# Kernel optimization log

Hardware: AMD Instinct MI355X
Metric: run time of the kernel (lower is better)

Reference implementation:

```python
import jax, jax.numpy as jnp
import numpy as np

D = 3            # input_ch (pos dims)
L = 16           # n_levels
F = 2            # n_feats per level
LOG2 = 19
CAP = 1 << LOG2  # hashmap capacity per level
COARSEST, FINEST = 16.0, 2048.0
N = 524288
D1 = D + 1
HASH_MULT = np.int32(2531011)


def _elevate_matrix():
    # Linear map R^D -> hyperplane {sum=0} in R^{D+1} (Adams et al. permutohedral lattice)
    sf = 1.0 / np.sqrt(np.arange(1, D + 1, dtype=np.float64) * np.arange(2, D + 2, dtype=np.float64))
    E = np.zeros((D1, D), np.float32)
    E[0, :] = sf
    for i in range(1, D1):
        E[i, i - 1] = -i * sf[i - 1]
        E[i, i:] = sf[i:]
    return E


def _scales():
    g = (FINEST / COARSEST) ** (np.arange(L, dtype=np.float64) / (L - 1))
    return (COARSEST * g).astype(np.float32)


def permuto_forward(pos, params):
    E = jnp.asarray(_elevate_matrix())
    scales = jnp.asarray(_scales())
    x = pos[None] * scales[:, None, None]              # [L,N,D]
    elev = jnp.einsum('vp,lnp->lnv', E, x)             # [L,N,D1]
    # nearest lattice remainder-0 point (multiples of D1)
    rem0f = jnp.round(elev / D1) * D1
    sums = (jnp.sum(rem0f, -1) / D1).astype(jnp.int32)  # exactly integer
    di = elev - rem0f
    # rank[i] = #{j : d_j > d_i  or (d_j == d_i and j < i)}
    gt = di[..., None, :] > di[..., :, None]
    eq = di[..., None, :] == di[..., :, None]
    jlt = jnp.arange(D1)[None, :] < jnp.arange(D1)[:, None]
    rank = jnp.sum(gt | (eq & jlt), -1).astype(jnp.int32) + sums[..., None]
    rem0 = rem0f.astype(jnp.int32)
    under = (rank < 0).astype(jnp.int32)
    over = (rank > D).astype(jnp.int32)
    rank = rank + (under - over) * D1
    rem0 = rem0 + (under - over) * D1
    # barycentric weights of the D1 simplex vertices
    delta = (elev - rem0.astype(elev.dtype)) / D1      # [L,N,D1]
    dbr = jnp.take_along_axis(delta, jnp.argsort(rank, -1), -1)  # delta ordered by rank
    w0 = 1.0 + dbr[..., -1] - dbr[..., 0]
    w = jnp.concatenate([w0[..., None], -(dbr[..., 1:] - dbr[..., :-1])[..., ::-1]], -1)  # [L,N,D1]
    # integer keys of the D1 simplex vertices (first D coords; last is implicit)
    kk = jnp.arange(D1, dtype=jnp.int32)
    keys = (rem0[..., None, :D] + kk[:, None]
            - D1 * (rank[..., None, :D] > (D - kk[:, None])).astype(jnp.int32))  # [L,N,D1,D]
    # hash: k = (k + key_i) * 2531011, wrap in 32 bits, mask to capacity (pow2)
    h = jnp.zeros(keys.shape[:-1], jnp.int32)
    for i in range(D):
        h = (h + keys[..., i]) * HASH_MULT
    idx = h & (CAP - 1)                                # [L,N,D1]
    flat_idx = idx + jnp.arange(L, dtype=jnp.int32)[:, None, None] * CAP
    feats = params.reshape(L * CAP, F)[flat_idx]       # [L,N,D1,F]
    out = jnp.einsum('lnv,lnvf->lnf', w, feats)        # [L,N,F]
    return jnp.moveaxis(out, 0, 1).reshape(pos.shape[0], L * F)


def setup_inputs() -> dict:
    key = jax.random.key(0)
    k1, k2 = jax.random.split(key)
    pos = jax.random.uniform(k1, (N, D), jnp.float32)                 # coords in [0,1)
    params = jax.random.normal(k2, (L * CAP * F,), jnp.float32) * 1e-4  # param_init std
    return {"input": pos, "flattened_params": params}


def reference(input, flattened_params):
    return permuto_forward(input, flattened_params)
```

## Files before the change

### kernel.cpp

```cpp
#include <hip/hip_runtime.h>
#include <hip/hip_fp16.h>
#include <cmath>

namespace {

typedef float    vf4 __attribute__((ext_vector_type(4)));
typedef unsigned uv2 __attribute__((ext_vector_type(2)));

constexpr int kN = 524288;
constexpr int kL = 16;
constexpr int kCapLog2 = 19;
constexpr int kCap = 1 << kCapLog2;
constexpr int kCapMask = kCap - 1;
constexpr unsigned kHashMult = 2531011u;

constexpr int cD[4][3]   = {{ 8, 8, 6},{10,10, 9},{13,12,10},{17,16,14}};
constexpr int cB[4][3]   = {{-4,-16,-16},{-4,-20,-24},{-4,-24,-28},{-4,-32,-40}};
constexpr int cCnt[4]    = {1536, 3600, 6240, 15232};
constexpr int cOff[4]    = {0, 1536, 5136, 11376};
constexpr int kLdsCnt    = 11376;
constexpr int kDenseCnt  = 26608;

struct ScaleArr { float s[kL]; };

__device__ __forceinline__ void permuto_point(
    float x0, float x1, float x2, int rem0[4], int rank[4], float w[4])
{
    const float E00 = (float)( 0.70710678118654752440);
    const float E01 = (float)( 0.40824829046386301637);
    const float E02 = (float)( 0.28867513459481288225);
    const float E10 = (float)(-0.70710678118654752440);
    const float E21 = (float)(-2.0 * 0.40824829046386301637);
    const float E32 = (float)(-3.0 * 0.28867513459481288225);

    float elev[4];
    elev[0] = E00 * x0 + E01 * x1 + E02 * x2;
    elev[1] = E10 * x0 + E01 * x1 + E02 * x2;
    elev[2] =            E21 * x1 + E02 * x2;
    elev[3] =                       E32 * x2;

    float rem0f[4], di[4];
    #pragma unroll
    for (int v = 0; v < 4; ++v) {
        rem0f[v] = rintf(elev[v] * 0.25f) * 4.0f;
        di[v]    = elev[v] - rem0f[v];
    }
    const int sums = (int)((((rem0f[0] + rem0f[1]) + rem0f[2]) + rem0f[3]) * 0.25f);

    #pragma unroll
    for (int a = 0; a < 4; ++a) {
        int r = 0;
        #pragma unroll
        for (int b = 0; b < 4; ++b)
            r += (di[b] > di[a]) || (di[b] == di[a] && b < a);
        rank[a] = r + sums;
        rem0[a] = (int)rem0f[a];
    }
    #pragma unroll
    for (int v = 0; v < 4; ++v) {
        if (rank[v] < 0)      { rank[v] += 4; rem0[v] += 4; }
        else if (rank[v] > 3) { rank[v] -= 4; rem0[v] -= 4; }
    }

    float dbr[4];
    #pragma unroll
    for (int v = 0; v < 4; ++v)
        dbr[rank[v] & 3] = (elev[v] - (float)rem0[v]) * 0.25f;

    w[0] = (1.0f + dbr[3]) - dbr[0];
    w[1] = dbr[2] - dbr[3];
    w[2] = dbr[1] - dbr[2];
    w[3] = dbr[0] - dbr[1];
}

__global__ __launch_bounds__(256) void conv_tab(const float* __restrict__ params,
                                                unsigned* __restrict__ tab)
{
    const int i = blockIdx.x * 256 + threadIdx.x;
    vf4 v = __builtin_nontemporal_load((const vf4*)params + i);
    __half2 a = __floats2half2_rn(v.x, v.y);
    __half2 b = __floats2half2_rn(v.z, v.w);
    uv2 o;
    o.x = *reinterpret_cast<unsigned*>(&a);
    o.y = *reinterpret_cast<unsigned*>(&b);
    __builtin_nontemporal_store(o, (uv2*)tab + i);
}

__global__ __launch_bounds__(256) void build_dense(const float* __restrict__ params,
                                                   unsigned* __restrict__ dense)
{
    const int e = blockIdx.x * 256 + threadIdx.x;
    if (e >= kDenseCnt) return;
    int l, r;
    if      (e < cOff[1]) { l = 0; r = e; }
    else if (e < cOff[2]) { l = 1; r = e - cOff[1]; }
    else if (e < cOff[3]) { l = 2; r = e - cOff[2]; }
    else                  { l = 3; r = e - cOff[3]; }
    const int d0 = cD[l][0], d1 = cD[l][1], d2 = cD[l][2];
    const int per = d0 * d1 * d2;
    const int k  = r / per;  r -= k * per;
    const int i0 = r / (d1 * d2); r -= i0 * (d1 * d2);
    const int i1 = r / d2;
    const int i2 = r - i1 * d2;

    const int key0 = cB[l][0] + 4 * i0 + k;
    const int key1 = cB[l][1] + 4 * i1 + k;
    const int key2 = cB[l][2] + 4 * i2 + k;
    int h = 0;
    h = (int)((unsigned)(h + key0) * kHashMult);
    h = (int)((unsigned)(h + key1) * kHashMult);
    h = (int)((unsigned)(h + key2) * kHashMult);
    const size_t entry = ((size_t)l << kCapLog2) + (h & kCapMask);
    const __half2 hv = __floats2half2_rn(params[entry * 2], params[entry * 2 + 1]);
    dense[e] = *reinterpret_cast<const unsigned*>(&hv);
}

__global__ __launch_bounds__(256) void permuto_coarse(
    const float* __restrict__ pos,
    const unsigned* __restrict__ dense,
    unsigned* __restrict__ out_t16,
    ScaleArr sc)
{
    __shared__ unsigned sd[kLdsCnt];
    for (int i = threadIdx.x; i < kLdsCnt; i += 256)
        sd[i] = dense[i];
    __syncthreads();

    const int n = blockIdx.x * 256 + threadIdx.x;
    const float p0 = __builtin_nontemporal_load(pos + 3 * n + 0);
    const float p1 = __builtin_nontemporal_load(pos + 3 * n + 1);
    const float p2 = __builtin_nontemporal_load(pos + 3 * n + 2);
    const unsigned* __restrict__ denseL3 = dense + cOff[3];

    #pragma unroll
    for (int l = 0; l < 4; ++l) {
        const float s = sc.s[l];
        int rem0[4], rank[4];
        float w[4];
        permuto_point(p0 * s, p1 * s, p2 * s, rem0, rank, w);

        unsigned ev[4];
        #pragma unroll
        for (int k = 0; k < 4; ++k) {
            const int i0 = (rem0[0] - 4 * (rank[0] > 3 - k) - cB[l][0]) >> 2;
            const int i1 = (rem0[1] - 4 * (rank[1] > 3 - k) - cB[l][1]) >> 2;
            const int i2 = (rem0[2] - 4 * (rank[2] > 3 - k) - cB[l][2]) >> 2;
            const int idx = ((k * cD[l][0] + i0) * cD[l][1] + i1) * cD[l][2] + i2;
            ev[k] = (l < 3) ? sd[cOff[l] + idx] : denseL3[idx];
        }
        float o0 = 0.0f, o1 = 0.0f;
        #pragma unroll
        for (int k = 0; k < 4; ++k) {
            const __half2 hv = *reinterpret_cast<const __half2*>(&ev[k]);
            o0 += w[k] * __low2float(hv);
            o1 += w[k] * __high2float(hv);
        }
        const __half2 po = __floats2half2_rn(o0, o1);
        __builtin_nontemporal_store(*reinterpret_cast<const unsigned*>(&po),
                                    out_t16 + ((size_t)l << kCapLog2) + n);
    }
}

__global__ __launch_bounds__(256) void permuto_fine(
    const float* __restrict__ pos,
    const unsigned* __restrict__ tab,
    unsigned* __restrict__ out_t16,
    ScaleArr sc)
{
    const int b   = blockIdx.x;
    const int xcd = b & 7;
    const int j   = b >> 3;
    int level, n;
    if (j < 2048) {
        level = 4 + xcd;
        n = (j << 8) + threadIdx.x;
    } else {
        level = 12 + (xcd & 3);
        const int c = ((j - 2048) << 1) | (xcd >> 2);
        n = (c << 8) + threadIdx.x;
    }

    const float s  = sc.s[level];
    const float x0 = __builtin_nontemporal_load(pos + 3 * n + 0) * s;
    const float x1 = __builtin_nontemporal_load(pos + 3 * n + 1) * s;
    const float x2 = __builtin_nontemporal_load(pos + 3 * n + 2) * s;

    int rem0[4], rank[4];
    float w[4];
    permuto_point(x0, x1, x2, rem0, rank, w);

    const unsigned* __restrict__ t = tab + ((size_t)level << kCapLog2);
    int hidx[4];
    #pragma unroll
    for (int k = 0; k < 4; ++k) {
        int h = 0;
        #pragma unroll
        for (int i = 0; i < 3; ++i) {
            const int key = rem0[i] + k - 4 * (rank[i] > 3 - k);
            h = (int)((unsigned)(h + key) * kHashMult);
        }
        hidx[k] = h & kCapMask;
    }
    unsigned e[4];
    #pragma unroll
    for (int k = 0; k < 4; ++k) e[k] = t[hidx[k]];

    float o0 = 0.0f, o1 = 0.0f;
    #pragma unroll
    for (int k = 0; k < 4; ++k) {
        const __half2 hv = *reinterpret_cast<const __half2*>(&e[k]);
        o0 += w[k] * __low2float(hv);
        o1 += w[k] * __high2float(hv);
    }
    const __half2 po = __floats2half2_rn(o0, o1);
    __builtin_nontemporal_store(*reinterpret_cast<const unsigned*>(&po),
                                out_t16 + ((size_t)level << kCapLog2) + n);
}

__global__ __launch_bounds__(256) void transpose_out16(
    const unsigned* __restrict__ out_t16, vf4* __restrict__ out4)
{
    __shared__ float tile[256][36];
    const int t  = threadIdx.x;
    const int p0 = blockIdx.x * 256;

    #pragma unroll
    for (int l = 0; l < kL; ++l) {
        const unsigned u = __builtin_nontemporal_load(out_t16 + ((size_t)l << kCapLog2) + p0 + t);
        const __half2 hv = *reinterpret_cast<const __half2*>(&u);
        tile[t][2 * l + 0] = __low2float(hv);
        tile[t][2 * l + 1] = __high2float(hv);
    }
    __syncthreads();

    const size_t base = (size_t)p0 * 8;
    #pragma unroll
    for (int i = 0; i < 8; ++i) {
        const int idx = i * 256 + t;
        const int p = idx >> 3, q = idx & 7;
        vf4 v = *reinterpret_cast<const vf4*>(&tile[p][4 * q]);
        out4[base + idx] = v;
    }
}

__global__ __launch_bounds__(256) void permuto_fwd(
    const float* __restrict__ pos,
    const float* __restrict__ params,
    float* __restrict__ out,
    ScaleArr sc)
{
    const int gid = blockIdx.x * 256 + threadIdx.x;
    const int l = gid & (kL - 1);
    const int n = gid >> 4;

    const float s  = sc.s[l];
    const float x0 = pos[3 * n + 0] * s;
    const float x1 = pos[3 * n + 1] * s;
    const float x2 = pos[3 * n + 2] * s;

    int rem0[4], rank[4];
    float w[4];
    permuto_point(x0, x1, x2, rem0, rank, w);

    const float2* __restrict__ tab = (const float2*)params + ((size_t)l << kCapLog2);
    float o0 = 0.0f, o1 = 0.0f;
    #pragma unroll
    for (int k = 0; k < 4; ++k) {
        int h = 0;
        #pragma unroll
        for (int i = 0; i < 3; ++i) {
            const int key = rem0[i] + k - 4 * (rank[i] > 3 - k);
            h = (int)((unsigned)(h + key) * kHashMult);
        }
        const float2 f = tab[h & kCapMask];
        o0 += w[k] * f.x;
        o1 += w[k] * f.y;
    }
    ((float2*)out)[(n << 4) + l] = make_float2(o0, o1);
}

}

extern "C" void kernel_launch(void* const* d_in, const int* in_sizes, int n_in,
                              void* d_out, int out_size, void* d_ws, size_t ws_size,
                              hipStream_t stream) {
    const float* pos    = (const float*)d_in[0];
    const float* params = (const float*)d_in[1];
    float* out          = (float*)d_out;

    ScaleArr sc;
    for (int l = 0; l < kL; ++l)
        sc.s[l] = (float)(16.0 * pow(128.0, (double)l / 15.0));

    const size_t tab_bytes   = (size_t)kL * kCap * 4;
    const size_t outt_bytes  = (size_t)kL * kN * 4;
    const size_t dense_bytes = (size_t)kDenseCnt * 4;

    if (ws_size >= tab_bytes + outt_bytes + dense_bytes) {
        unsigned* tab     = (unsigned*)d_ws;
        unsigned* out_t16 = (unsigned*)((char*)d_ws + tab_bytes);
        unsigned* dense   = (unsigned*)((char*)d_ws + tab_bytes + outt_bytes);

        conv_tab<<<(kL * kCap * 2 / 4) / 256, 256, 0, stream>>>(params, tab);
        build_dense<<<(kDenseCnt + 255) / 256, 256, 0, stream>>>(params, dense);
        permuto_coarse<<<kN / 256, 256, 0, stream>>>(pos, dense, out_t16, sc);
        permuto_fine<<<8 * 3072, 256, 0, stream>>>(pos, tab, out_t16, sc);
        transpose_out16<<<kN / 256, 256, 0, stream>>>(out_t16, (vf4*)out);
    } else {
        permuto_fwd<<<(kN * kL) / 256, 256, 0, stream>>>(pos, params, out, sc);
    }
}
```

Before: 186.3 us.

## Fuse table conversion with fp32 gathers for levels 4-6 into one kernel

```diff
diff --git a/kernel.cpp b/kernel.cpp
--- a/kernel.cpp
+++ b/kernel.cpp
@@ -16,10 +16,13 @@
 
 constexpr int cD[4][3]   = {{ 8, 8, 6},{10,10, 9},{13,12,10},{17,16,14}};
 constexpr int cB[4][3]   = {{-4,-16,-16},{-4,-20,-24},{-4,-24,-28},{-4,-32,-40}};
-constexpr int cCnt[4]    = {1536, 3600, 6240, 15232};
 constexpr int cOff[4]    = {0, 1536, 5136, 11376};
 constexpr int kLdsCnt    = 11376;
 constexpr int kDenseCnt  = 26608;
+
+constexpr int kMegaMain  = 15360;
+constexpr int kBuildBlks = 104;
+constexpr int kConvBaseF4 = 7 * (kCap * 2 / 4);
 
 struct ScaleArr { float s[kL]; };
 
@@ -73,46 +76,149 @@
     w[3] = dbr[0] - dbr[1];
 }
 
-__global__ __launch_bounds__(256) void conv_tab(const float* __restrict__ params,
-                                                unsigned* __restrict__ tab)
-{
-    const int i = blockIdx.x * 256 + threadIdx.x;
-    vf4 v = __builtin_nontemporal_load((const vf4*)params + i);
-    __half2 a = __floats2half2_rn(v.x, v.y);
-    __half2 b = __floats2half2_rn(v.z, v.w);
-    uv2 o;
-    o.x = *reinterpret_cast<unsigned*>(&a);
-    o.y = *reinterpret_cast<unsigned*>(&b);
-    __builtin_nontemporal_store(o, (uv2*)tab + i);
-}
-
-__global__ __launch_bounds__(256) void build_dense(const float* __restrict__ params,
-                                                   unsigned* __restrict__ dense)
-{
-    const int e = blockIdx.x * 256 + threadIdx.x;
-    if (e >= kDenseCnt) return;
-    int l, r;
-    if      (e < cOff[1]) { l = 0; r = e; }
-    else if (e < cOff[2]) { l = 1; r = e - cOff[1]; }
-    else if (e < cOff[3]) { l = 2; r = e - cOff[2]; }
-    else                  { l = 3; r = e - cOff[3]; }
-    const int d0 = cD[l][0], d1 = cD[l][1], d2 = cD[l][2];
-    const int per = d0 * d1 * d2;
-    const int k  = r / per;  r -= k * per;
-    const int i0 = r / (d1 * d2); r -= i0 * (d1 * d2);
-    const int i1 = r / d2;
-    const int i2 = r - i1 * d2;
-
-    const int key0 = cB[l][0] + 4 * i0 + k;
-    const int key1 = cB[l][1] + 4 * i1 + k;
-    const int key2 = cB[l][2] + 4 * i2 + k;
-    int h = 0;
-    h = (int)((unsigned)(h + key0) * kHashMult);
-    h = (int)((unsigned)(h + key1) * kHashMult);
-    h = (int)((unsigned)(h + key2) * kHashMult);
-    const size_t entry = ((size_t)l << kCapLog2) + (h & kCapMask);
-    const __half2 hv = __floats2half2_rn(params[entry * 2], params[entry * 2 + 1]);
-    dense[e] = *reinterpret_cast<const unsigned*>(&hv);
+__global__ __launch_bounds__(256) void mega1(
+    const float* __restrict__ pos,
+    const float* __restrict__ params,
+    unsigned* __restrict__ tab,
+    unsigned* __restrict__ out_t16,
+    unsigned* __restrict__ dense,
+    ScaleArr sc)
+{
+    const int b = blockIdx.x;
+    if (b < kMegaMain) {
+        const int q = b / 5, r = b % 5;
+        if (r < 2) {
+            const int idx   = q * 2 + r;
+            const int level = 4 + (idx >> 11);
+            const int n     = ((idx & 2047) << 8) + threadIdx.x;
+
+            const float s  = sc.s[level];
+            const float x0 = __builtin_nontemporal_load(pos + 3 * n + 0) * s;
+            const float x1 = __builtin_nontemporal_load(pos + 3 * n + 1) * s;
+            const float x2 = __builtin_nontemporal_load(pos + 3 * n + 2) * s;
+
+            int rem0[4], rank[4];
+            float w[4];
+            permuto_point(x0, x1, x2, rem0, rank, w);
+
+            const float2* __restrict__ t2 =
+                (const float2*)params + ((size_t)level << kCapLog2);
+            int hidx[4];
+            #pragma unroll
+            for (int k = 0; k < 4; ++k) {
+                int h = 0;
+                #pragma unroll
+                for (int i = 0; i < 3; ++i) {
+                    const int key = rem0[i] + k - 4 * (rank[i] > 3 - k);
+                    h = (int)((unsigned)(h + key) * kHashMult);
+                }
+                hidx[k] = h & kCapMask;
+            }
+            float2 f[4];
+            #pragma unroll
+            for (int k = 0; k < 4; ++k) f[k] = t2[hidx[k]];
+
+            float o0 = 0.0f, o1 = 0.0f;
+            #pragma unroll
+            for (int k = 0; k < 4; ++k) { o0 += w[k] * f[k].x; o1 += w[k] * f[k].y; }
+
+            const __half2 po = __floats2half2_rn(o0, o1);
+            __builtin_nontemporal_store(*reinterpret_cast<const unsigned*>(&po),
+                                        out_t16 + ((size_t)level << kCapLog2) + n);
+        } else {
+            const int i  = q * 3 + (r - 2);
+            const int jj = kConvBaseF4 + i * 256 + threadIdx.x;
+            vf4 v = __builtin_nontemporal_load((const vf4*)params + jj);
+            __half2 a = __floats2half2_rn(v.x, v.y);
+            __half2 c = __floats2half2_rn(v.z, v.w);
+            uv2 o;
+            o.x = *reinterpret_cast<unsigned*>(&a);
+            o.y = *reinterpret_cast<unsigned*>(&c);
+            __builtin_nontemporal_store(o, (uv2*)tab + jj);
+        }
+    } else {
+        const int e = (b - kMegaMain) * 256 + threadIdx.x;
+        if (e >= kDenseCnt) return;
+        int l, r;
+        if      (e < cOff[1]) { l = 0; r = e; }
+        else if (e < cOff[2]) { l = 1; r = e - cOff[1]; }
+        else if (e < cOff[3]) { l = 2; r = e - cOff[2]; }
+        else                  { l = 3; r = e - cOff[3]; }
+        const int d0 = cD[l][0], d1 = cD[l][1], d2 = cD[l][2];
+        const int per = d0 * d1 * d2;
+        int rr = r;
+        const int k  = rr / per;  rr -= k * per;
+        const int i0 = rr / (d1 * d2); rr -= i0 * (d1 * d2);
+        const int i1 = rr / d2;
+        const int i2 = rr - i1 * d2;
+
+        const int key0 = cB[l][0] + 4 * i0 + k;
+        const int key1 = cB[l][1] + 4 * i1 + k;
+        const int key2 = cB[l][2] + 4 * i2 + k;
+        int h = 0;
+        h = (int)((unsigned)(h + key0) * kHashMult);
+        h = (int)((unsigned)(h + key1) * kHashMult);
+        h = (int)((unsigned)(h + key2) * kHashMult);
+        const size_t entry = ((size_t)l << kCapLog2) + (h & kCapMask);
+        const __half2 hv = __floats2half2_rn(params[entry * 2], params[entry * 2 + 1]);
+        dense[e] = *reinterpret_cast<const unsigned*>(&hv);
+    }
+}
+
+__global__ __launch_bounds__(256) void fine715(
+    const float* __restrict__ pos,
+    const unsigned* __restrict__ tab,
+    unsigned* __restrict__ out_t16,
+    ScaleArr sc)
+{
+    const int b   = blockIdx.x;
+    const int xcd = b & 7;
+    const int j   = b >> 3;
+    int level, n;
+    if (j < 2048) {
+        level = 7 + xcd;
+        n = (j << 8) + threadIdx.x;
+    } else {
+        level = 15;
+        const int c = (j - 2048) + (xcd << 8);
+        n = (c << 8) + threadIdx.x;
+    }
+
+    const float s  = sc.s[level];
+    const float x0 = __builtin_nontemporal_load(pos + 3 * n + 0) * s;
+    const float x1 = __builtin_nontemporal_load(pos + 3 * n + 1) * s;
+    const float x2 = __builtin_nontemporal_load(pos + 3 * n + 2) * s;
+
+    int rem0[4], rank[4];
+    float w[4];
+    permuto_point(x0, x1, x2, rem0, rank, w);
+
+    const unsigned* __restrict__ t = tab + ((size_t)level << kCapLog2);
+    int hidx[4];
+    #pragma unroll
+    for (int k = 0; k < 4; ++k) {
+        int h = 0;
+        #pragma unroll
+        for (int i = 0; i < 3; ++i) {
+            const int key = rem0[i] + k - 4 * (rank[i] > 3 - k);
+            h = (int)((unsigned)(h + key) * kHashMult);
+        }
+        hidx[k] = h & kCapMask;
+    }
+    unsigned e[4];
+    #pragma unroll
+    for (int k = 0; k < 4; ++k) e[k] = t[hidx[k]];
+
+    float o0 = 0.0f, o1 = 0.0f;
+    #pragma unroll
+    for (int k = 0; k < 4; ++k) {
+        const __half2 hv = *reinterpret_cast<const __half2*>(&e[k]);
+        o0 += w[k] * __low2float(hv);
+        o1 += w[k] * __high2float(hv);
+    }
+    const __half2 po = __floats2half2_rn(o0, o1);
+    __builtin_nontemporal_store(*reinterpret_cast<const unsigned*>(&po),
+                                out_t16 + ((size_t)level << kCapLog2) + n);
 }
 
 __global__ __launch_bounds__(256) void permuto_coarse(
@@ -161,62 +267,6 @@
     }
 }
 
-__global__ __launch_bounds__(256) void permuto_fine(
-    const float* __restrict__ pos,
-    const unsigned* __restrict__ tab,
-    unsigned* __restrict__ out_t16,
-    ScaleArr sc)
-{
-    const int b   = blockIdx.x;
-    const int xcd = b & 7;
-    const int j   = b >> 3;
-    int level, n;
-    if (j < 2048) {
-        level = 4 + xcd;
-        n = (j << 8) + threadIdx.x;
-    } else {
-        level = 12 + (xcd & 3);
-        const int c = ((j - 2048) << 1) | (xcd >> 2);
-        n = (c << 8) + threadIdx.x;
-    }
-
-    const float s  = sc.s[level];
-    const float x0 = __builtin_nontemporal_load(pos + 3 * n + 0) * s;
-    const float x1 = __builtin_nontemporal_load(pos + 3 * n + 1) * s;
-    const float x2 = __builtin_nontemporal_load(pos + 3 * n + 2) * s;
-
-    int rem0[4], rank[4];
-    float w[4];
-    permuto_point(x0, x1, x2, rem0, rank, w);
-
-    const unsigned* __restrict__ t = tab + ((size_t)level << kCapLog2);
-    int hidx[4];
-    #pragma unroll
-    for (int k = 0; k < 4; ++k) {
-        int h = 0;
-        #pragma unroll
-        for (int i = 0; i < 3; ++i) {
-            const int key = rem0[i] + k - 4 * (rank[i] > 3 - k);
-            h = (int)((unsigned)(h + key) * kHashMult);
-        }
-        hidx[k] = h & kCapMask;
-    }
-    unsigned e[4];
-    #pragma unroll
-    for (int k = 0; k < 4; ++k) e[k] = t[hidx[k]];
-
-    float o0 = 0.0f, o1 = 0.0f;
-    #pragma unroll
-    for (int k = 0; k < 4; ++k) {
-        const __half2 hv = *reinterpret_cast<const __half2*>(&e[k]);
-        o0 += w[k] * __low2float(hv);
-        o1 += w[k] * __high2float(hv);
-    }
-    const __half2 po = __floats2half2_rn(o0, o1);
-    __builtin_nontemporal_store(*reinterpret_cast<const unsigned*>(&po),
-                                out_t16 + ((size_t)level << kCapLog2) + n);
-}
-
 __global__ __launch_bounds__(256) void transpose_out16(
     const unsigned* __restrict__ out_t16, vf4* __restrict__ out4)
 {
@@ -301,10 +351,9 @@
         unsigned* out_t16 = (unsigned*)((char*)d_ws + tab_bytes);
         unsigned* dense   = (unsigned*)((char*)d_ws + tab_bytes + outt_bytes);
 
-        conv_tab<<<(kL * kCap * 2 / 4) / 256, 256, 0, stream>>>(params, tab);
-        build_dense<<<(kDenseCnt + 255) / 256, 256, 0, stream>>>(params, dense);
+        mega1<<<kMegaMain + kBuildBlks, 256, 0, stream>>>(pos, params, tab, out_t16, dense, sc);
+        fine715<<<8 * 2304, 256, 0, stream>>>(pos, tab, out_t16, sc);
         permuto_coarse<<<kN / 256, 256, 0, stream>>>(pos, dense, out_t16, sc);
-        permuto_fine<<<8 * 3072, 256, 0, stream>>>(pos, tab, out_t16, sc);
         transpose_out16<<<kN / 256, 256, 0, stream>>>(out_t16, (vf4*)out);
     } else {
         permuto_fwd<<<(kN * kL) / 256, 256, 0, stream>>>(pos, params, out, sc);
```

Measured after the change: 175.1 us. -6.0%, faster.
